# Performance work log

Hardware: AMD Instinct MI355X
Metric: run time of the kernel (lower is better)

## Reference

```python
import jax, jax.numpy as jnp
import numpy as np

B, L, FD = 16, 196, 2048      # batch, fmap locations (14x14), resnet101 feat dim
N, WD, HD, DD = 1000, 300, 512, 5  # n_class, word_dim, hid_dim, d_dim
E, TMAX, NIMG = 50000, 5, 1000     # n_edges, gru steps, imagenet classes


def setup_inputs():
    key = jax.random.key(0)
    ks = jax.random.split(key, 32)
    p = lambda k, s: (jax.random.normal(k, s, jnp.float32) * 0.02)
    z = lambda n: jnp.zeros((n,), jnp.float32)
    return {
        'feats': jax.random.normal(ks[0], (B, L, FD), jnp.float32),
        'embed': jax.random.normal(ks[1], (N, WD), jnp.float32),
        'edges': jax.random.randint(ks[2], (2, E), 0, N, jnp.int32),
        # attention key/query nets
        'W_key': p(ks[3], (FD, HD)), 'b_key': z(HD),
        'W_query': p(ks[4], (WD, HD)), 'b_query': z(HD),
        # F_in: feat_dim -> 512 -> d_dim (relu)
        'Wf1': p(ks[5], (FD, 512)), 'bf1': z(512),
        'Wf2': p(ks[6], (512, DD)), 'bf2': z(DD),
        # F_rel: 2*word_dim -> 256 -> 1 (relu)
        'Wr1': p(ks[7], (2 * WD, 256)), 'br1': z(256),
        'Wr2': p(ks[8], (256, 1)), 'br2': z(1),
        # F_out: d_dim -> 512 -> 1 (relu)
        'Wo1': p(ks[9], (DD, 512)), 'bo1': z(512),
        'Wo2': p(ks[10], (512, 1)), 'bo2': z(1),
        # GRUCell (torch layout: [3*d, d] stacked r,z,n)
        'W_ih': p(ks[11], (3 * DD, DD)), 'b_ih': z(3 * DD),
        'W_hh': p(ks[12], (3 * DD, DD)), 'b_hh': z(3 * DD),
        # imagenet classifier on pooled features
        'W_clf': p(ks[13], (FD, NIMG)), 'b_clf': z(NIMG),
    }


def _gru_cell(x, h, W_ih, W_hh, b_ih, b_hh):
    gi = x @ W_ih.T + b_ih            # [M, 3d]
    gh = h @ W_hh.T + b_hh
    i_r, i_z, i_n = jnp.split(gi, 3, axis=-1)
    h_r, h_z, h_n = jnp.split(gh, 3, axis=-1)
    r = jax.nn.sigmoid(i_r + h_r)
    zg = jax.nn.sigmoid(i_z + h_z)
    n = jnp.tanh(i_n + r * h_n)
    return (1.0 - zg) * n + zg * h


def reference(feats, embed, edges, W_key, b_key, W_query, b_query,
              Wf1, bf1, Wf2, bf2, Wr1, br1, Wr2, br2, Wo1, bo1, Wo2, bo2,
              W_ih, b_ih, W_hh, b_hh, W_clf, b_clf):
    # imagenet scores from globally pooled backbone features
    pooled = jnp.mean(feats, axis=1)                      # [B, FD]
    imgnet_scores = jax.nn.softmax(pooled @ W_clf + b_clf, axis=1)

    # label-conditional spatial attention
    keys = feats @ W_key + b_key                          # [B, L, HD]
    queries = embed @ W_query + b_query                   # [N, HD]
    scores = jnp.einsum('blh,nh->bnl', keys, queries)     # [B, N, L]
    attn = jax.nn.softmax(scores, axis=2)
    graph_input = jnp.einsum('bnl,blf->bnf', attn, feats) # [B, N, FD]
    graph_input = graph_input.reshape(-1, FD)             # [B*N, FD]

    # F_in MLP -> initial hidden state
    h0 = jax.nn.relu(graph_input @ Wf1 + bf1) @ Wf2 + bf2  # [B*N, DD]

    # edge weights from word-embedding pairs, scattered into dense [N, N]
    et = jnp.concatenate([embed[edges[0]], embed[edges[1]]], axis=1)  # [E, 2*WD]
    vals = jnp.tanh((jax.nn.relu(et @ Wr1 + br1) @ Wr2 + br2).reshape(-1))
    prop_mat = jnp.zeros((N, N), jnp.float32).at[edges[0], edges[1]].add(vals)

    # t_max message-passing + GRU steps (sequential recurrence)
    def step(hidden, _):
        msg = jnp.tanh(jnp.einsum('nm,bmd->bnd', prop_mat,
                                  hidden.reshape(B, N, DD))).reshape(-1, DD)
        return _gru_cell(msg, hidden, W_ih, W_hh, b_ih, b_hh), None
    hidden, _ = jax.lax.scan(step, h0, None, length=TMAX)

    logits = (jax.nn.relu(hidden @ Wo1 + bo1) @ Wo2 + bo2).reshape(B, N)
    return logits, attn, imgnet_scores
```

## Files before the change

kernel.cpp:

```cpp
#include <hip/hip_runtime.h>
#include <hip/hip_bf16.h>
#include <math.h>

#define B_   16
#define L_   196
#define FD_  2048
#define N_   1000
#define WD_  300
#define HD_  512
#define DD_  5
#define E_   50000
#define TMAX_ 5
#define NIMG_ 1000
#define WDP_ 320
#define LP_  224
#define EKP_ 640

typedef __attribute__((ext_vector_type(8))) short bf16x8;
typedef __attribute__((ext_vector_type(4))) float f32x4;

#define SMEM_MEGA1    49152
#define SMEM_MM_SPLIT 49152
#define SMEM_MM_NS    24576
#define SMEM_PREP     4352

#define SBAR()    asm volatile("s_barrier" ::: "memory")
#define WVM(N)    asm volatile("s_waitcnt vmcnt(" #N ")" ::: "memory")

__device__ __forceinline__ short bf_hi(float x) {
    unsigned u = __float_as_uint(x);
    unsigned r = u + 0x7fffu + ((u >> 16) & 1u);
    return (short)(r >> 16);
}
__device__ __forceinline__ float bf2f_(short s) {
    return __uint_as_float(((unsigned)(unsigned short)s) << 16);
}

__device__ __forceinline__ void gl16(const short* g, char* l) {
    __builtin_amdgcn_global_load_lds(
        (const __attribute__((address_space(1))) void*)g,
        (__attribute__((address_space(3))) void*)l, 16, 0, 0);
}

#define OUT_SPLIT 1
#define OUT_SC    2
#define OUT_F1T   3
#define OUT_H0    4

template<int OUTMODE, bool SPLIT>
__device__ __forceinline__ void mm_core(
    char* sm, int bx, int by, int zb,
    const short* __restrict__ Ah, const short* __restrict__ Al,
    const short* __restrict__ Bh, const short* __restrict__ Bl,
    const float* __restrict__ bias, void* __restrict__ C0, void* __restrict__ C1,
    void* __restrict__ C2, const float* __restrict__ W2,
    int M, int N, int K, int kbeg, int kend)
{
    const int PBUF = SPLIT ? 24576 : 12288;
    char* AsH = sm;
    char* AsL = sm + 8192;
    char* BsH = sm + (SPLIT ? 16384 : 8192);
    char* BsL = sm + 20480;
    int t = threadIdx.x;
    int lane = t & 63, w = t >> 6;
    int q = lane >> 4, r = lane & 15;
    int row0 = by * 128, col0 = bx * 64;

    int srow = t >> 2, cd = t & 3;
    int cg = cd ^ ((srow >> 1) & 3);
    int gA0 = row0 + srow;       if (gA0 >= M) gA0 = M - 1;
    int gA1 = row0 + 64 + srow;  if (gA1 >= M) gA1 = M - 1;
    int gB  = col0 + srow;       if (gB  >= N) gB  = N - 1;
    const short* pA0 = Ah + (long)gA0 * K + cg * 8 + kbeg;
    const short* pA1 = Ah + (long)gA1 * K + cg * 8 + kbeg;
    const short* pB  = Bh + (long)gB  * K + cg * 8 + kbeg;
    const short* pA0l = Ah; const short* pA1l = Ah; const short* pBl = Bh;
    if (SPLIT) {
        pA0l = Al + (long)gA0 * K + cg * 8 + kbeg;
        pA1l = Al + (long)gA1 * K + cg * 8 + kbeg;
        pBl  = Bl + (long)gB  * K + cg * 8 + kbeg;
    }
    char* dA0 = AsH + t * 16;
    char* dA1 = AsH + 4096 + t * 16;
    char* dB  = BsH + t * 16;
    char* dA0l = AsL + t * 16;
    char* dA1l = AsL + 4096 + t * 16;
    char* dBl  = BsL + t * 16;

    int x = (q ^ ((r >> 1) & 3)) * 16;
    int aoff0 = (w * 32 + r) * 64 + x;
    int aoff1 = aoff0 + 1024;
    int boff[4];
    #pragma unroll
    for (int ct = 0; ct < 4; ct++) boff[ct] = (ct * 16 + r) * 64 + x;

    f32x4 zero4 = {0.f, 0.f, 0.f, 0.f};
    f32x4 acc[2][4];
    #pragma unroll
    for (int i = 0; i < 2; i++)
        #pragma unroll
        for (int j = 0; j < 4; j++) acc[i][j] = zero4;

    auto stage = [&](int ks) {
        int off = (ks & 1) * PBUF;
        int ko = ks * 32;
        gl16(pA0 + ko, dA0 + off);
        gl16(pA1 + ko, dA1 + off);
        gl16(pB  + ko, dB  + off);
        if (SPLIT) {
            gl16(pA0l + ko, dA0l + off);
            gl16(pA1l + ko, dA1l + off);
            gl16(pBl  + ko, dBl  + off);
        }
    };

    int nk = (kend - kbeg) >> 5;
    stage(0);
    for (int ks = 0; ks < nk; ks++) {
        if (ks + 1 < nk) {
            stage(ks + 1);
            if (SPLIT) { WVM(6); } else { WVM(3); }
        } else {
            WVM(0);
        }
        SBAR();

        int cur = (ks & 1) * PBUF;
        bf16x8 ah0 = *(const bf16x8*)(AsH + cur + aoff0);
        bf16x8 ah1 = *(const bf16x8*)(AsH + cur + aoff1);
        bf16x8 al0, al1;
        if (SPLIT) {
            al0 = *(const bf16x8*)(AsL + cur + aoff0);
            al1 = *(const bf16x8*)(AsL + cur + aoff1);
        }
        #pragma unroll
        for (int ct = 0; ct < 4; ct++) {
            bf16x8 bh = *(const bf16x8*)(BsH + cur + boff[ct]);
            acc[0][ct] = __builtin_amdgcn_mfma_f32_16x16x32_bf16(ah0, bh, acc[0][ct], 0, 0, 0);
            acc[1][ct] = __builtin_amdgcn_mfma_f32_16x16x32_bf16(ah1, bh, acc[1][ct], 0, 0, 0);
            if (SPLIT) {
                acc[0][ct] = __builtin_amdgcn_mfma_f32_16x16x32_bf16(al0, bh, acc[0][ct], 0, 0, 0);
                acc[1][ct] = __builtin_amdgcn_mfma_f32_16x16x32_bf16(al1, bh, acc[1][ct], 0, 0, 0);
                bf16x8 bl = *(const bf16x8*)(BsL + cur + boff[ct]);
                acc[0][ct] = __builtin_amdgcn_mfma_f32_16x16x32_bf16(ah0, bl, acc[0][ct], 0, 0, 0);
                acc[1][ct] = __builtin_amdgcn_mfma_f32_16x16x32_bf16(ah1, bl, acc[1][ct], 0, 0, 0);
            }
        }
        if (ks + 1 < nk) SBAR();
    }

    if (OUTMODE == OUT_H0) {
        float s[2][4][DD_];
        #pragma unroll
        for (int i = 0; i < 2; i++)
            #pragma unroll
            for (int reg = 0; reg < 4; reg++)
                #pragma unroll
                for (int d = 0; d < DD_; d++) s[i][reg][d] = 0.f;
        #pragma unroll
        for (int i = 0; i < 2; i++) {
            #pragma unroll
            for (int ct = 0; ct < 4; ct++) {
                int n = col0 + ct * 16 + r;
                float w2v[DD_];
                #pragma unroll
                for (int d = 0; d < DD_; d++) w2v[d] = W2[n * DD_ + d];
                float b1 = bias[n];
                #pragma unroll
                for (int reg = 0; reg < 4; reg++) {
                    int m = row0 + w * 32 + i * 16 + q * 4 + reg;
                    if (m >= M) continue;
                    float val = fmaxf(acc[i][ct][reg] + b1, 0.f);
                    #pragma unroll
                    for (int d = 0; d < DD_; d++) s[i][reg][d] = fmaf(val, w2v[d], s[i][reg][d]);
                }
            }
        }
        #pragma unroll
        for (int i = 0; i < 2; i++)
            #pragma unroll
            for (int reg = 0; reg < 4; reg++)
                #pragma unroll
                for (int d = 0; d < DD_; d++) {
                    float v = s[i][reg][d];
                    v += __shfl_xor(v, 1);
                    v += __shfl_xor(v, 2);
                    v += __shfl_xor(v, 4);
                    v += __shfl_xor(v, 8);
                    if (r == 0) {
                        int m = row0 + w * 32 + i * 16 + q * 4 + reg;
                        if (m < M)
                            atomicAdd(&((float*)C0)[(long)m * (B_ * DD_) + zb * DD_ + d], v);
                    }
                }
        return;
    }

    #pragma unroll
    for (int i = 0; i < 2; i++) {
        #pragma unroll
        for (int ct = 0; ct < 4; ct++) {
            #pragma unroll
            for (int reg = 0; reg < 4; reg++) {
                int m = row0 + w * 32 + i * 16 + q * 4 + reg;
                int n = col0 + ct * 16 + r;
                if (m >= M || n >= N) continue;
                float v = acc[i][ct][reg];
                if (OUTMODE == OUT_SC) {
                    ((float*)C0)[(long)m * N + n] = v;
                } else if (OUTMODE == OUT_F1T) {
                    int b = m / 196, l = m - b * 196;
                    ((short*)C2)[((long)b * 512 + n) * LP_ + l] = bf_hi(v);
                } else {
                    float v2 = v + bias[n];
                    long idx = (long)m * N + n;
                    short hi = bf_hi(v2);
                    ((short*)C0)[idx] = hi;
                    ((short*)C1)[idx] = bf_hi(v2 - bf2f_(hi));
                }
            }
        }
    }
}

__device__ __forceinline__ void edge_core(
    char* sm, int be,
    const short* __restrict__ embedH, const int* __restrict__ edges,
    const short* __restrict__ Wr1T, const float* __restrict__ br1,
    const float* __restrict__ Wr2, const float* __restrict__ br2,
    float* __restrict__ prop)
{
    const int EPBUF = 20480;
    char* As = sm;
    char* Bs = sm + 4096;
    int* src = (int*)(sm + 40960);
    int* dst = (int*)(sm + 41216);
    float (*part)[5] = (float(*)[5])(sm + 41472);
    int t = threadIdx.x;
    int e0 = be * 64;
    if (t < 64) {
        int e = e0 + t;
        src[t] = (e < E_) ? edges[e] : 0;
        dst[t] = (e < E_) ? edges[E_ + e] : 0;
    }
    __syncthreads();
    int lane = t & 63, w = t >> 6, q = lane >> 4, r = lane & 15;
    f32x4 zero4 = {0.f, 0.f, 0.f, 0.f};
    f32x4 acc[4][4];
    #pragma unroll
    for (int i = 0; i < 4; i++)
        #pragma unroll
        for (int j = 0; j < 4; j++) acc[i][j] = zero4;

    int srow = t >> 2, cd = t & 3;
    int cg = cd ^ ((srow >> 1) & 3);
    const short* baseS = embedH + (long)src[srow] * WDP_ + cg * 8;
    const short* baseD = embedH + (long)dst[srow] * WDP_ + cg * 8;
    const short* pB = Wr1T + (long)srow * EKP_ + cg * 8;
    char* dA = As + t * 16;
    char* dB = Bs + t * 16;

    int x = (q ^ ((r >> 1) & 3)) * 16;
    int aoff[4], boff[4];
    #pragma unroll
    for (int i = 0; i < 4; i++) {
        aoff[i] = (i * 16 + r) * 64 + x;
        boff[i] = (w * 64 + i * 16 + r) * 64 + x;
    }

    auto estage = [&](int ks) {
        int off = (ks & 1) * EPBUF;
        const short* pa = (ks < 10) ? baseS + ks * 32 : baseD + (ks - 10) * 32;
        gl16(pa, dA + off);
        #pragma unroll
        for (int i = 0; i < 4; i++)
            gl16(pB + (long)i * 64 * EKP_ + ks * 32, dB + i * 4096 + off);
    };

    estage(0);
    for (int ks = 0; ks < 20; ks++) {
        if (ks + 1 < 20) {
            estage(ks + 1);
            WVM(5);
        } else {
            WVM(0);
        }
        SBAR();

        int cur = (ks & 1) * EPBUF;
        bf16x8 af[4], bfr[4];
        #pragma unroll
        for (int rt = 0; rt < 4; rt++) af[rt] = *(const bf16x8*)(As + cur + aoff[rt]);
        #pragma unroll
        for (int ct = 0; ct < 4; ct++) bfr[ct] = *(const bf16x8*)(Bs + cur + boff[ct]);
        #pragma unroll
        for (int rt = 0; rt < 4; rt++)
            #pragma unroll
            for (int ct = 0; ct < 4; ct++)
                acc[rt][ct] = __builtin_amdgcn_mfma_f32_16x16x32_bf16(af[rt], bfr[ct], acc[rt][ct], 0, 0, 0);
        if (ks + 1 < 20) SBAR();
    }
    float b1v[4], w2v[4];
    #pragma unroll
    for (int ct = 0; ct < 4; ct++) {
        int u = w * 64 + ct * 16 + r;
        b1v[ct] = br1[u];
        w2v[ct] = Wr2[u];
    }
    #pragma unroll
    for (int rt = 0; rt < 4; rt++) {
        #pragma unroll
        for (int reg = 0; reg < 4; reg++) {
            float s = 0.f;
            #pragma unroll
            for (int ct = 0; ct < 4; ct++)
                s = fmaf(fmaxf(acc[rt][ct][reg] + b1v[ct], 0.f), w2v[ct], s);
            s += __shfl_xor(s, 1);
            s += __shfl_xor(s, 2);
            s += __shfl_xor(s, 4);
            s += __shfl_xor(s, 8);
            if (r == 0) part[rt * 16 + q * 4 + reg][w] = s;
        }
    }
    __syncthreads();
    if (t < 64 && e0 + t < E_) {
        float s = part[t][0] + part[t][1] + part[t][2] + part[t][3];
        atomicAdd(&prop[(long)src[t] * N_ + dst[t]], tanhf(s + br2[0]));
    }
}

__device__ __forceinline__ void transconv_core(
    char* sm, int bx, int by,
    const float* __restrict__ in, short* __restrict__ outH, short* __restrict__ outL,
    int Kd, int N, int Ks)
{
    float (*tile)[33] = (float(*)[33])sm;
    int k0 = bx * 32, n0 = by * 32;
    int t = threadIdx.x;
    int tr = t >> 5, tc = t & 31;
    #pragma unroll
    for (int i = 0; i < 4; i++) {
        int k = k0 + tr + i * 8, n = n0 + tc;
        tile[tr + i * 8][tc] = (k < Kd && n < N) ? in[(long)k * N + n] : 0.f;
    }
    __syncthreads();
    #pragma unroll
    for (int i = 0; i < 4; i++) {
        int n = n0 + tr + i * 8, k = k0 + tc;
        if (n < N && k < Ks) {
            float x = tile[tc][tr + i * 8];
            short hi = bf_hi(x);
            outH[(long)n * Ks + k] = hi;
            if (outL) outL[(long)n * Ks + k] = bf_hi(x - bf2f_(hi));
        }
    }
}

__global__ __launch_bounds__(256) void prep(
    float* __restrict__ prop, float* __restrict__ Ht0, const float* __restrict__ bf2,
    const float* __restrict__ feats, float* __restrict__ pooled,
    short* __restrict__ featsH, short* __restrict__ featsL,
    const float* __restrict__ embed, short* __restrict__ embH, short* __restrict__ embL,
    const float* __restrict__ W_key, const float* __restrict__ Wf1,
    short* __restrict__ WkfH, short* __restrict__ WkfL,
    const float* __restrict__ W_query, short* __restrict__ WqTh, short* __restrict__ WqTl,
    const float* __restrict__ Wr1, short* __restrict__ Wr1T, short* __restrict__ F1T)
{
    __shared__ __align__(16) char sm[SMEM_PREP];
    int b = blockIdx.x, t = threadIdx.x;
    if (b < 977) {
        int i = (b * 256 + t) * 4;
        if (i < N_ * N_) { float4 z = {0.f, 0.f, 0.f, 0.f}; *(float4*)(prop + i) = z; }
    } else if (b < 1290) {
        int i = (b - 977) * 256 + t;
        if (i < N_ * B_ * DD_) Ht0[i] = bf2[i % DD_];
    } else if (b < 1322) {
        int idx = (b - 1290) * 256 + t;
        int bb = idx >> 9, f4 = (idx & 511) * 4;
        const float* p = feats + (long)bb * L_ * FD_ + f4;
        float4 acc = {0.f, 0.f, 0.f, 0.f};
        for (int l = 0; l < L_; l++) {
            float4 v = *(const float4*)(p + (long)l * FD_);
            acc.x += v.x; acc.y += v.y; acc.z += v.z; acc.w += v.w;
        }
        const float inv = 1.0f / L_;
        acc.x *= inv; acc.y *= inv; acc.z *= inv; acc.w *= inv;
        *(float4*)(pooled + (long)bb * FD_ + f4) = acc;
    } else if (b < 4458) {
        long i = ((long)(b - 1322) * 256 + t) * 8;
        float4 v0 = *(const float4*)(feats + i);
        float4 v1 = *(const float4*)(feats + i + 4);
        float xs[8] = {v0.x, v0.y, v0.z, v0.w, v1.x, v1.y, v1.z, v1.w};
        short h[8], l8[8];
        #pragma unroll
        for (int j = 0; j < 8; j++) {
            h[j] = bf_hi(xs[j]);
            l8[j] = bf_hi(xs[j] - bf2f_(h[j]));
        }
        *(int4*)(featsH + i) = *(int4*)h;
        *(int4*)(featsL + i) = *(int4*)l8;
    } else if (b < 4771) {
        int i = ((b - 4458) * 256 + t) * 4;
        if (i < N_ * WDP_) {
            int n = i / WDP_, c = i - n * WDP_;
            short h[4], l4[4];
            if (c < WD_) {
                float4 v = *(const float4*)(embed + (long)n * WD_ + c);
                float xs[4] = {v.x, v.y, v.z, v.w};
                #pragma unroll
                for (int j = 0; j < 4; j++) {
                    h[j] = bf_hi(xs[j]);
                    l4[j] = bf_hi(xs[j] - bf2f_(h[j]));
                }
            } else {
                #pragma unroll
                for (int j = 0; j < 4; j++) { h[j] = 0; l4[j] = 0; }
            }
            *(int2*)(embH + (long)n * WDP_ + c) = *(int2*)h;
            *(int2*)(embL + (long)n * WDP_ + c) = *(int2*)l4;
        }
    } else if (b < 5795) {
        int bb = b - 4771;
        transconv_core(sm, bb % 64, bb / 64, W_key, WkfH, WkfL, FD_, HD_, FD_);
    } else if (b < 6819) {
        int bb = b - 5795;
        transconv_core(sm, bb % 64, bb / 64, Wf1, WkfH + (size_t)512 * FD_, nullptr, FD_, HD_, FD_);
    } else if (b < 6979) {
        int bb = b - 6819;
        transconv_core(sm, bb % 10, bb / 10, W_query, WqTh, WqTl, WD_, HD_, WDP_);
    } else if (b < 7139) {
        int bb = b - 6979;
        int bx = bb % 20, by = bb / 20;
        float (*tile)[33] = (float(*)[33])sm;
        int k0 = bx * 32, n0 = by * 32;
        int tr = t >> 5, tc = t & 31;
        #pragma unroll
        for (int i = 0; i < 4; i++) {
            int kout = k0 + tr + i * 8, n = n0 + tc;
            int kin = (kout < 320) ? kout : kout - 20;
            bool valid = (kout < 320) ? (kout < 300) : (kout < 620);
            tile[tr + i * 8][tc] = valid ? Wr1[(long)kin * 256 + n] : 0.f;
        }
        __syncthreads();
        #pragma unroll
        for (int i = 0; i < 4; i++) {
            int n = n0 + tr + i * 8, k = k0 + tc;
            Wr1T[(long)n * EKP_ + k] = bf_hi(tile[tc][tr + i * 8]);
        }
    } else {
        int idx = (b - 7139) * 256 + t;
        int row = idx / 7, j = idx - row * 7;
        int2 z2; z2.x = 0; z2.y = 0;
        *(int2*)(F1T + (long)row * LP_ + 196 + j * 4) = z2;
    }
}

__global__ __launch_bounds__(256) void mega1(
    const short* __restrict__ featsH, const short* __restrict__ featsL,
    const short* __restrict__ WkfH, const short* __restrict__ WkfL,
    const float* __restrict__ b_key, short* __restrict__ keysH, short* __restrict__ keysL,
    short* __restrict__ F1T,
    const short* __restrict__ embH, const short* __restrict__ embL,
    const short* __restrict__ WqTh, const short* __restrict__ WqTl,
    const float* __restrict__ b_query, short* __restrict__ qH, short* __restrict__ qL,
    const int* __restrict__ edges, const short* __restrict__ Wr1T,
    const float* __restrict__ br1, const float* __restrict__ Wr2,
    const float* __restrict__ br2, float* __restrict__ prop,
    const float* __restrict__ pooled, const float* __restrict__ W_clf,
    const float* __restrict__ b_clf, float* __restrict__ Pimg)
{
    __shared__ __align__(16) char sm[SMEM_MEGA1];
    int b = blockIdx.x;
    if (b < 200) {
        int l = (b & 7) * 25 + (b >> 3);
        mm_core<OUT_SPLIT, true>(sm, l & 7, l >> 3, 0,
            featsH, featsL, WkfH, WkfL, b_key,
            keysH, keysL, nullptr, nullptr, B_ * L_, 512, FD_, 0, FD_);
    } else if (b < 400) {
        int bb = b - 200;
        int l = (bb & 7) * 25 + (bb >> 3);
        mm_core<OUT_F1T, false>(sm, l & 7, l >> 3, 0,
            featsH, nullptr, WkfH + (size_t)512 * FD_, nullptr, nullptr,
            nullptr, nullptr, F1T, nullptr, B_ * L_, 512, FD_, 0, FD_);
    } else if (b < 464) {
        int bb = b - 400;
        int l = (bb & 7) * 8 + (bb >> 3);
        mm_core<OUT_SPLIT, true>(sm, l & 7, l >> 3, 0,
            embH, embL, WqTh, WqTl, b_query,
            qH, qL, nullptr, nullptr, N_, HD_, WDP_, 0, WDP_);
    } else if (b < 1246) {
        edge_core(sm, b - 464, embH, edges, Wr1T, br1, Wr2, br2, prop);
    } else {
        int bb = b - 1246;
        int ks = bb >> 2, nb = bb & 3;
        float* poolLds = (float*)sm;
        int t = threadIdx.x;
        for (int id = t; id < 1024; id += 256) {
            int bi = id >> 6, koff = (id & 63) * 4;
            *(float4*)&poolLds[bi * 256 + koff] =
                *(const float4*)(pooled + (long)bi * FD_ + ks * 256 + koff);
        }
        __syncthreads();
        int n = nb * 256 + t;
        if (n < NIMG_) {
            float acc[16];
            #pragma unroll
            for (int bi = 0; bi < 16; bi++) acc[bi] = 0.f;
            #pragma unroll 4
            for (int k = 0; k < 256; k++) {
                float wv = W_clf[(long)(ks * 256 + k) * NIMG_ + n];
                #pragma unroll
                for (int bi = 0; bi < 16; bi++)
                    acc[bi] = fmaf(poolLds[bi * 256 + k], wv, acc[bi]);
            }
            float bc = (ks == 0) ? b_clf[n] : 0.f;
            #pragma unroll
            for (int bi = 0; bi < 16; bi++)
                Pimg[(long)ks * (B_ * NIMG_) + bi * NIMG_ + n] = acc[bi] + bc;
        }
    }
}

__global__ __launch_bounds__(256) void mega2(
    const short* __restrict__ qH, const short* __restrict__ qL,
    const short* __restrict__ keysH, const short* __restrict__ keysL,
    float* __restrict__ Pattn,
    const float* __restrict__ Pimg, float* __restrict__ out_img)
{
    __shared__ __align__(16) char sm[SMEM_MM_SPLIT];
    int b = blockIdx.x;
    if (b < 512) {
        int l = (b & 7) * 64 + (b >> 3);
        int zb = l >> 5, by = (l >> 2) & 7, bx = l & 3;
        const short* Bh = keysH + (long)zb * L_ * HD_;
        const short* Bl = keysL + (long)zb * L_ * HD_;
        float* C0 = Pattn + (long)zb * N_ * L_;
        mm_core<OUT_SC, true>(sm, bx, by, 0, qH, qL, Bh, Bl, nullptr,
                              C0, nullptr, nullptr, nullptr,
                              N_, L_, HD_, 0, HD_);
    } else {
        int t = threadIdx.x;
        int wave = (b - 512) * 4 + (t >> 6), lane = t & 63;
        if (wave >= B_) return;
        const int PER = (NIMG_ + 63) / 64;
        float v[PER];
        float m = -1e30f;
        int cnt = 0;
        for (int k = lane; k < NIMG_; k += 64) {
            float s = 0.f;
            #pragma unroll
            for (int ks = 0; ks < 8; ks++) s += Pimg[(long)ks * (B_ * NIMG_) + wave * NIMG_ + k];
            v[cnt] = s; m = fmaxf(m, s); cnt++;
        }
        #pragma unroll
        for (int off = 32; off; off >>= 1) m = fmaxf(m, __shfl_xor(m, off));
        float s = 0.f;
        for (int i = 0; i < cnt; i++) { v[i] = expf(v[i] - m); s += v[i]; }
        #pragma unroll
        for (int off = 32; off; off >>= 1) s += __shfl_xor(s, off);
        float inv = 1.f / s;
        cnt = 0;
        for (int k = lane; k < NIMG_; k += 64) out_img[(long)wave * NIMG_ + k] = v[cnt++] * inv;
    }
}

__global__ void softmax_attn(const float* __restrict__ P0,
                             float* __restrict__ X, short* __restrict__ Xb, int rows)
{
    int gid = blockIdx.x * blockDim.x + threadIdx.x;
    int wave = gid >> 6, lane = gid & 63;
    if (wave >= rows) return;
    const int PER = (L_ + 63) / 64;
    float v[PER];
    float m = -1e30f;
    int cnt = 0;
    for (int k = lane; k < L_; k += 64) {
        v[cnt] = P0[(long)wave * L_ + k];
        m = fmaxf(m, v[cnt]); cnt++;
    }
    #pragma unroll
    for (int off = 32; off; off >>= 1) m = fmaxf(m, __shfl_xor(m, off));
    float s = 0.f;
    for (int i = 0; i < cnt; i++) { v[i] = expf(v[i] - m); s += v[i]; }
    #pragma unroll
    for (int off = 32; off; off >>= 1) s += __shfl_xor(s, off);
    float inv = 1.f / s;
    cnt = 0;
    for (int k = lane; k < L_; k += 64) {
        float val = v[cnt++] * inv;
        X[(long)wave * L_ + k] = val;
        Xb[(long)wave * LP_ + k] = bf_hi(val);
    }
    if (lane < LP_ - L_) Xb[(long)wave * LP_ + L_ + lane] = 0;
}

__global__ __launch_bounds__(256) void h0gemm(
    const short* __restrict__ attnH, const short* __restrict__ F1T,
    const float* __restrict__ bf1, const float* __restrict__ Wf2,
    float* __restrict__ Ht0)
{
    __shared__ __align__(16) char sm[SMEM_MM_NS];
    int b = blockIdx.x;
    int l = (b & 7) * 128 + (b >> 3);
    int zb = l >> 6, by = (l >> 3) & 7, bx = l & 7;
    const short* Ap = attnH + (long)zb * N_ * LP_;
    const short* Bp = F1T + (long)zb * HD_ * LP_;
    mm_core<OUT_H0, false>(sm, bx, by, zb, Ap, nullptr, Bp, nullptr,
                           bf1, Ht0, nullptr, nullptr, Wf2,
                           N_, HD_, LP_, 0, LP_);
}

__global__ __launch_bounds__(320) void step_kernel(
    const float* __restrict__ prop, const float* __restrict__ Hin,
    float* __restrict__ Hout,
    const float* __restrict__ W_ih, const float* __restrict__ b_ih,
    const float* __restrict__ W_hh, const float* __restrict__ b_hh)
{
    __shared__ float hinLds[100][80];
    __shared__ float propLds[4][100];
    __shared__ float msg[4][80];
    int t = threadIdx.x;
    int nl = t / 80, c = t - nl * 80;
    float a0 = 0.f, a1 = 0.f, a2 = 0.f, a3 = 0.f;
    for (int ch = 0; ch < 10; ch++) {
        int m0 = ch * 100;
        for (int id = t; id < 2000; id += 320) {
            int m = id / 20, coff = (id % 20) * 4;
            *(float4*)&hinLds[m][coff] = *(const float4*)(Hin + (long)(m0 + m) * 80 + coff);
        }
        if (t < 100) {
            int pn = t / 25, poff = (t % 25) * 4;
            *(float4*)&propLds[pn][poff] =
                *(const float4*)(prop + (long)(blockIdx.x * 4 + pn) * N_ + m0 + poff);
        }
        __syncthreads();
        #pragma unroll 5
        for (int m4 = 0; m4 < 100; m4 += 4) {
            a0 = fmaf(propLds[nl][m4 + 0], hinLds[m4 + 0][c], a0);
            a1 = fmaf(propLds[nl][m4 + 1], hinLds[m4 + 1][c], a1);
            a2 = fmaf(propLds[nl][m4 + 2], hinLds[m4 + 2][c], a2);
            a3 = fmaf(propLds[nl][m4 + 3], hinLds[m4 + 3][c], a3);
        }
        __syncthreads();
    }
    msg[nl][c] = tanhf((a0 + a1) + (a2 + a3));
    __syncthreads();
    if (t < 64) {
        int nl2 = t >> 4, b = t & 15;
        int n2 = blockIdx.x * 4 + nl2;
        float xv[DD_], h[DD_];
        #pragma unroll
        for (int j = 0; j < DD_; j++) {
            xv[j] = msg[nl2][b * DD_ + j];
            h[j] = Hin[(long)n2 * 80 + b * DD_ + j];
        }
        float gi[3 * DD_], gh[3 * DD_];
        #pragma unroll
        for (int g = 0; g < 3 * DD_; g++) {
            float a = b_ih[g], cc = b_hh[g];
            #pragma unroll
            for (int k = 0; k < DD_; k++) {
                a = fmaf(xv[k], W_ih[g * DD_ + k], a);
                cc = fmaf(h[k], W_hh[g * DD_ + k], cc);
            }
            gi[g] = a; gh[g] = cc;
        }
        #pragma unroll
        for (int j = 0; j < DD_; j++) {
            float rr = 1.f / (1.f + expf(-(gi[j] + gh[j])));
            float zz = 1.f / (1.f + expf(-(gi[DD_ + j] + gh[DD_ + j])));
            float nn2 = tanhf(gi[2 * DD_ + j] + rr * gh[2 * DD_ + j]);
            Hout[(long)n2 * 80 + b * DD_ + j] = (1.f - zz) * nn2 + zz * h[j];
        }
    }
}

__global__ __launch_bounds__(256) void out_kernel(
    const float* __restrict__ ht, const float* __restrict__ Wo1,
    const float* __restrict__ bo1, const float* __restrict__ Wo2,
    const float* __restrict__ bo2, float* __restrict__ logits, int rows)
{
    __shared__ float w1[DD_][HD_];
    __shared__ float w2[HD_];
    __shared__ float b1[HD_];
    int t = threadIdx.x;
    for (int j = t; j < HD_; j += 256) {
        w2[j] = Wo2[j];
        b1[j] = bo1[j];
        #pragma unroll
        for (int d = 0; d < DD_; d++) w1[d][j] = Wo1[d * HD_ + j];
    }
    __syncthreads();
    int wv = t >> 6, lane = t & 63;
    float bo2v = bo2[0];
    #pragma unroll
    for (int rr = 0; rr < 16; rr++) {
        int row = blockIdx.x * 64 + wv * 16 + rr;
        if (row >= rows) break;
        int b = row / N_, n = row - b * N_;
        float x[DD_];
        #pragma unroll
        for (int i = 0; i < DD_; i++) x[i] = ht[(long)n * (B_ * DD_) + b * DD_ + i];
        float acc = 0.f;
        for (int j = lane; j < HD_; j += 64) {
            float h = b1[j];
            #pragma unroll
            for (int d = 0; d < DD_; d++) h = fmaf(x[d], w1[d][j], h);
            h = fmaxf(h, 0.f);
            acc = fmaf(h, w2[j], acc);
        }
        #pragma unroll
        for (int off = 32; off; off >>= 1) acc += __shfl_down(acc, off);
        if (lane == 0) logits[row] = acc + bo2v;
    }
}

extern "C" void kernel_launch(void* const* d_in, const int* in_sizes, int n_in,
                              void* d_out, int out_size, void* d_ws, size_t ws_size,
                              hipStream_t stream)
{
    const float* feats   = (const float*)d_in[0];
    const float* embed   = (const float*)d_in[1];
    const int*   edges   = (const int*)  d_in[2];
    const float* W_key   = (const float*)d_in[3];
    const float* b_key   = (const float*)d_in[4];
    const float* W_query = (const float*)d_in[5];
    const float* b_query = (const float*)d_in[6];
    const float* Wf1     = (const float*)d_in[7];
    const float* bf1     = (const float*)d_in[8];
    const float* Wf2     = (const float*)d_in[9];
    const float* bf2     = (const float*)d_in[10];
    const float* Wr1     = (const float*)d_in[11];
    const float* br1     = (const float*)d_in[12];
    const float* Wr2     = (const float*)d_in[13];
    const float* br2     = (const float*)d_in[14];
    const float* Wo1     = (const float*)d_in[15];
    const float* bo1     = (const float*)d_in[16];
    const float* Wo2     = (const float*)d_in[17];
    const float* bo2     = (const float*)d_in[18];
    const float* W_ih    = (const float*)d_in[19];
    const float* b_ih    = (const float*)d_in[20];
    const float* W_hh    = (const float*)d_in[21];
    const float* b_hh    = (const float*)d_in[22];
    const float* W_clf   = (const float*)d_in[23];
    const float* b_clf   = (const float*)d_in[24];

    float* out_logits = (float*)d_out;
    float* out_attn   = out_logits + B_ * N_;
    float* out_img    = out_attn + (long)B_ * N_ * L_;

    char* p = (char*)d_ws;
    auto alloc = [&](size_t bytes) { void* r = (void*)p; p += (bytes + 255) & ~(size_t)255; return r; };
    float* pooled  = (float*)alloc((size_t)B_ * FD_ * 4);
    short* featsH  = (short*)alloc((size_t)B_ * L_ * FD_ * 2);
    short* featsL  = (short*)alloc((size_t)B_ * L_ * FD_ * 2);
    short* WkfH    = (short*)alloc((size_t)1024 * FD_ * 2);
    short* WkfL    = (short*)alloc((size_t)512 * FD_ * 2);
    short* WqTh    = (short*)alloc((size_t)HD_ * WDP_ * 2);
    short* WqTl    = (short*)alloc((size_t)HD_ * WDP_ * 2);
    short* Wr1T    = (short*)alloc((size_t)256 * EKP_ * 2);
    short* embH    = (short*)alloc((size_t)N_ * WDP_ * 2);
    short* embL    = (short*)alloc((size_t)N_ * WDP_ * 2);
    short* keysH   = (short*)alloc((size_t)B_ * L_ * HD_ * 2);
    short* keysL   = (short*)alloc((size_t)B_ * L_ * HD_ * 2);
    short* qH      = (short*)alloc((size_t)N_ * HD_ * 2);
    short* qL      = (short*)alloc((size_t)N_ * HD_ * 2);
    short* attnH   = (short*)alloc((size_t)B_ * N_ * LP_ * 2);
    short* F1T     = (short*)alloc((size_t)B_ * HD_ * LP_ * 2);
    float* prop    = (float*)alloc((size_t)N_ * N_ * 4);
    float* Ht0     = (float*)alloc((size_t)N_ * B_ * DD_ * 4);
    float* Ht1     = (float*)alloc((size_t)N_ * B_ * DD_ * 4);
    float* Pimg    = (float*)alloc((size_t)8 * B_ * NIMG_ * 4);
    float* Pattn   = (float*)alloc((size_t)B_ * N_ * L_ * 4);

    prep<<<7363, 256, 0, stream>>>(prop, Ht0, bf2, feats, pooled, featsH, featsL,
                                   embed, embH, embL, W_key, Wf1, WkfH, WkfL,
                                   W_query, WqTh, WqTl, Wr1, Wr1T, F1T);

    mega1<<<1278, 256, 0, stream>>>(featsH, featsL, WkfH, WkfL, b_key, keysH, keysL, F1T,
                                    embH, embL, WqTh, WqTl, b_query, qH, qL,
                                    edges, Wr1T, br1, Wr2, br2, prop,
                                    pooled, W_clf, b_clf, Pimg);

    mega2<<<516, 256, 0, stream>>>(qH, qL, keysH, keysL, Pattn, Pimg, out_img);

    softmax_attn<<<(B_ * N_ * 64 + 255) / 256, 256, 0, stream>>>(
        Pattn, out_attn, attnH, B_ * N_);

    h0gemm<<<1024, 256, 0, stream>>>(attnH, F1T, bf1, Wf2, Ht0);

    {
        float* hin = Ht0;
        float* hout = Ht1;
        for (int step = 0; step < TMAX_; step++) {
            step_kernel<<<N_ / 4, 320, 0, stream>>>(prop, hin, hout,
                                                    W_ih, b_ih, W_hh, b_hh);
            float* tmp = hin; hin = hout; hout = tmp;
        }
        out_kernel<<<250, 256, 0, stream>>>(hin, Wo1, bo1, Wo2, bo2,
                                            out_logits, B_ * N_);
    }
}
```

Baseline: 517.9 us.

## Split step-kernel reduction across two halves and flatten imagenet classifier blocks

Result: faster. 448.9 us, median of 2 (-13.3%).

```diff
diff --git a/kernel.cpp b/kernel.cpp
--- a/kernel.cpp
+++ b/kernel.cpp
@@ -492,31 +492,16 @@
         edge_core(sm, b - 464, embH, edges, Wr1T, br1, Wr2, br2, prop);
     } else {
         int bb = b - 1246;
-        int ks = bb >> 2, nb = bb & 3;
-        float* poolLds = (float*)sm;
-        int t = threadIdx.x;
-        for (int id = t; id < 1024; id += 256) {
-            int bi = id >> 6, koff = (id & 63) * 4;
-            *(float4*)&poolLds[bi * 256 + koff] =
-                *(const float4*)(pooled + (long)bi * FD_ + ks * 256 + koff);
-        }
-        __syncthreads();
-        int n = nb * 256 + t;
-        if (n < NIMG_) {
-            float acc[16];
-            #pragma unroll
-            for (int bi = 0; bi < 16; bi++) acc[bi] = 0.f;
+        int ks = bb / 63, ix = bb % 63;
+        int i = ix * 256 + threadIdx.x;
+        if (i < B_ * NIMG_) {
+            int bi = i / NIMG_, n = i % NIMG_;
+            const float* p = pooled + (long)bi * FD_ + ks * 256;
+            const float* w = W_clf + (long)(ks * 256) * NIMG_ + n;
+            float acc = (ks == 0) ? b_clf[n] : 0.f;
             #pragma unroll 4
-            for (int k = 0; k < 256; k++) {
-                float wv = W_clf[(long)(ks * 256 + k) * NIMG_ + n];
-                #pragma unroll
-                for (int bi = 0; bi < 16; bi++)
-                    acc[bi] = fmaf(poolLds[bi * 256 + k], wv, acc[bi]);
-            }
-            float bc = (ks == 0) ? b_clf[n] : 0.f;
-            #pragma unroll
-            for (int bi = 0; bi < 16; bi++)
-                Pimg[(long)ks * (B_ * NIMG_) + bi * NIMG_ + n] = acc[bi] + bc;
+            for (int k = 0; k < 256; k++) acc = fmaf(p[k], w[(long)k * NIMG_], acc);
+            Pimg[(long)ks * (B_ * NIMG_) + i] = acc;
         }
     }
 }
@@ -610,40 +595,34 @@
                            N_, HD_, LP_, 0, LP_);
 }
 
-__global__ __launch_bounds__(320) void step_kernel(
+__global__ __launch_bounds__(640) void step_kernel(
     const float* __restrict__ prop, const float* __restrict__ Hin,
     float* __restrict__ Hout,
     const float* __restrict__ W_ih, const float* __restrict__ b_ih,
     const float* __restrict__ W_hh, const float* __restrict__ b_hh)
 {
-    __shared__ float hinLds[100][80];
-    __shared__ float propLds[4][100];
-    __shared__ float msg[4][80];
+    __shared__ float msg[2][4][80];
     int t = threadIdx.x;
-    int nl = t / 80, c = t - nl * 80;
+    int half = t / 320, tt = t - half * 320;
+    int nl = tt / 80, c = tt - nl * 80;
+    int n = blockIdx.x * 4 + nl;
+    const float* pr = prop + (long)n * N_ + half * 500;
+    const float* hc = Hin + c + (long)half * 500 * 80;
     float a0 = 0.f, a1 = 0.f, a2 = 0.f, a3 = 0.f;
-    for (int ch = 0; ch < 10; ch++) {
-        int m0 = ch * 100;
-        for (int id = t; id < 2000; id += 320) {
-            int m = id / 20, coff = (id % 20) * 4;
-            *(float4*)&hinLds[m][coff] = *(const float4*)(Hin + (long)(m0 + m) * 80 + coff);
-        }
-        if (t < 100) {
-            int pn = t / 25, poff = (t % 25) * 4;
-            *(float4*)&propLds[pn][poff] =
-                *(const float4*)(prop + (long)(blockIdx.x * 4 + pn) * N_ + m0 + poff);
-        }
-        __syncthreads();
-        #pragma unroll 5
-        for (int m4 = 0; m4 < 100; m4 += 4) {
-            a0 = fmaf(propLds[nl][m4 + 0], hinLds[m4 + 0][c], a0);
-            a1 = fmaf(propLds[nl][m4 + 1], hinLds[m4 + 1][c], a1);
-            a2 = fmaf(propLds[nl][m4 + 2], hinLds[m4 + 2][c], a2);
-            a3 = fmaf(propLds[nl][m4 + 3], hinLds[m4 + 3][c], a3);
-        }
-        __syncthreads();
-    }
-    msg[nl][c] = tanhf((a0 + a1) + (a2 + a3));
+    #pragma unroll 4
+    for (int m4 = 0; m4 < 500; m4 += 4) {
+        float4 pv = *(const float4*)(pr + m4);
+        a0 = fmaf(pv.x, hc[(long)(m4 + 0) * 80], a0);
+        a1 = fmaf(pv.y, hc[(long)(m4 + 1) * 80], a1);
+        a2 = fmaf(pv.z, hc[(long)(m4 + 2) * 80], a2);
+        a3 = fmaf(pv.w, hc[(long)(m4 + 3) * 80], a3);
+    }
+    msg[half][nl][c] = (a0 + a1) + (a2 + a3);
+    __syncthreads();
+    if (t < 320) {
+        int nl2 = t / 80, c2 = t - nl2 * 80;
+        msg[0][nl2][c2] = tanhf(msg[0][nl2][c2] + msg[1][nl2][c2]);
+    }
     __syncthreads();
     if (t < 64) {
         int nl2 = t >> 4, b = t & 15;
@@ -651,7 +630,7 @@
         float xv[DD_], h[DD_];
         #pragma unroll
         for (int j = 0; j < DD_; j++) {
-            xv[j] = msg[nl2][b * DD_ + j];
+            xv[j] = msg[0][nl2][b * DD_ + j];
             h[j] = Hin[(long)n2 * 80 + b * DD_ + j];
         }
         float gi[3 * DD_], gh[3 * DD_];
@@ -777,7 +756,7 @@
                                    embed, embH, embL, W_key, Wf1, WkfH, WkfL,
                                    W_query, WqTh, WqTl, Wr1, Wr1T, F1T);
 
-    mega1<<<1278, 256, 0, stream>>>(featsH, featsL, WkfH, WkfL, b_key, keysH, keysL, F1T,
+    mega1<<<1750, 256, 0, stream>>>(featsH, featsL, WkfH, WkfL, b_key, keysH, keysL, F1T,
                                     embH, embL, WqTh, WqTl, b_query, qH, qL,
                                     edges, Wr1T, br1, Wr2, br2, prop,
                                     pooled, W_clf, b_clf, Pimg);
@@ -793,7 +772,7 @@
         float* hin = Ht0;
         float* hout = Ht1;
         for (int step = 0; step < TMAX_; step++) {
-            step_kernel<<<N_ / 4, 320, 0, stream>>>(prop, hin, hout,
+            step_kernel<<<N_ / 4, 640, 0, stream>>>(prop, hin, hout,
                                                     W_ih, b_ih, W_hh, b_hh);
             float* tmp = hin; hin = hout; hout = tmp;
         }
```
